# Optimization experiments

Measured on AMD Instinct MI355X. Metric: run time of the kernel, lower is better.

## Reference

```python
import jax, jax.numpy as jnp
import numpy as np

N, E, DIM, NF, ED = 15000, 30000, 64, 3, 1

def _gru_cell(x, h, w_ih, w_hh, b_ih, b_hh):
    gi = x @ w_ih.T + b_ih
    gh = h @ w_hh.T + b_hh
    ir, iz, i_n = jnp.split(gi, 3, axis=-1)
    hr, hz, hn = jnp.split(gh, 3, axis=-1)
    r = jax.nn.sigmoid(ir + hr)
    z = jax.nn.sigmoid(iz + hz)
    n = jnp.tanh(i_n + r * hn)
    return (1.0 - z) * n + z * h

def _lstm_cell(x, h, c, w_ih, w_hh, b_ih, b_hh):
    g = x @ w_ih.T + b_ih + h @ w_hh.T + b_hh
    i, f, gg, o = jnp.split(g, 4, axis=-1)
    c2 = jax.nn.sigmoid(f) * c + jax.nn.sigmoid(i) * jnp.tanh(gg)
    return jax.nn.sigmoid(o) * jnp.tanh(c2), c2

def setup_inputs():
    key = jax.random.key(0)
    ks = jax.random.split(key, 32)
    p = lambda k, shape: jax.random.normal(k, shape, jnp.float32) * 0.05
    return {
        "x": jax.random.normal(ks[0], (N, NF), jnp.float32),
        "edge_index": jax.random.randint(ks[1], (2, E), 0, N),
        "edge_attr": jax.random.uniform(ks[2], (E, ED), jnp.float32),
        "lin0_w": p(ks[3], (DIM, NF)), "lin0_b": p(ks[4], (DIM,)),
        "e1_w": p(ks[5], (DIM, ED)), "e1_b": p(ks[6], (DIM,)),
        "e2_w": p(ks[7], (DIM * DIM, DIM)), "e2_b": p(ks[8], (DIM * DIM,)),
        "root_w": p(ks[9], (DIM, DIM)), "conv_b": p(ks[10], (DIM,)),
        "gru_w_ih": p(ks[11], (3 * DIM, DIM)), "gru_w_hh": p(ks[12], (3 * DIM, DIM)),
        "gru_b_ih": p(ks[13], (3 * DIM,)), "gru_b_hh": p(ks[14], (3 * DIM,)),
        "s2s_w_ih": p(ks[15], (4 * DIM, 2 * DIM)), "s2s_w_hh": p(ks[16], (4 * DIM, DIM)),
        "s2s_b_ih": p(ks[17], (4 * DIM,)), "s2s_b_hh": p(ks[18], (4 * DIM,)),
        "mem_w_ih": p(ks[19], (4 * DIM, 2 * DIM)), "mem_w_hh": p(ks[20], (4 * DIM, DIM)),
        "mem_b_ih": p(ks[21], (4 * DIM,)), "mem_b_hh": p(ks[22], (4 * DIM,)),
        "lin1_w": p(ks[23], (DIM, DIM)), "lin1_b": p(ks[24], (DIM,)),
        "lin3_w": p(ks[25], (1, DIM)), "lin3_b": p(ks[26], (1,)),
    }

def reference(x, edge_index, edge_attr, lin0_w, lin0_b, e1_w, e1_b, e2_w, e2_b,
              root_w, conv_b, gru_w_ih, gru_w_hh, gru_b_ih, gru_b_hh,
              s2s_w_ih, s2s_w_hh, s2s_b_ih, s2s_b_hh,
              mem_w_ih, mem_w_hh, mem_b_ih, mem_b_hh,
              lin1_w, lin1_b, lin3_w, lin3_b):
    n = x.shape[0]
    src, dst = edge_index[0], edge_index[1]
    # per-edge weight matrices from the edge MLP: [E, DIM, DIM] (edge_attr is constant across the 6 conv steps)
    he = jax.nn.relu(edge_attr @ e1_w.T + e1_b)
    We = (he @ e2_w.T + e2_b).reshape(-1, DIM, DIM)
    deg = jax.ops.segment_sum(jnp.ones(src.shape[0], jnp.float32), dst, num_segments=n)
    denom = jnp.maximum(deg, 1.0)[:, None]
    out = jax.nn.relu(x @ lin0_w.T + lin0_b)   # [N, DIM]
    h = out                                    # GRU hidden init = lin0 output
    for _ in range(6):
        msg = jnp.einsum('ei,eio->eo', out[src], We)          # gather + per-edge matmul
        agg = jax.ops.segment_sum(msg, dst, num_segments=n) / denom  # mean aggr
        m = jax.nn.relu(agg + out @ root_w + conv_b)          # NNConv root + bias
        h = _gru_cell(m, h, gru_w_ih, gru_w_hh, gru_b_ih, gru_b_hh)
        out = h
    # Set2Set pooling over a single graph (data.batch is all zeros)
    q_star = jnp.zeros((1, 2 * DIM), x.dtype)
    hs = jnp.zeros((1, DIM), x.dtype)
    cs = jnp.zeros((1, DIM), x.dtype)
    for _ in range(6):
        hs, cs = _lstm_cell(q_star, hs, cs, s2s_w_ih, s2s_w_hh, s2s_b_ih, s2s_b_hh)
        e = out @ hs[0]                     # [N] attention logits
        a = jax.nn.softmax(e)
        r = (a[:, None] * out).sum(0, keepdims=True)  # [1, DIM]
        q_star = jnp.concatenate([hs, r], axis=-1)     # [1, 2*DIM]
    hx, cx = _lstm_cell(q_star, jnp.zeros((1, DIM), x.dtype), jnp.zeros((1, DIM), x.dtype),
                        mem_w_ih, mem_w_hh, mem_b_ih, mem_b_hh)
    o = jax.nn.relu(hx @ lin1_w.T + lin1_b)
    v = o @ lin3_w.T + lin3_b               # [1, 1]
    return v, hx, cx
```

## Files before the change

### kernel.cpp

```cpp
#include <hip/hip_runtime.h>
#include <math.h>

#define Nn 15000
#define NP 15008
#define Ee 30000
#define NB_E 118
#define EB 938

#define OFF_AGG   0
#define OFF_DEG   960512
#define ZERO_END  975520
#define OFF_OUT   975520
#define OFF_DINV  1936032
#define OFF_AT    1951040
#define OFF_BT    2217280
#define OFF_BP    2483520
#define OFF_U     2483584
#define OFF_V     2487744
#define OFF_MC    2491904
#define OFF_PE    2491920
#define OFF_BH    2521920
#define OFF_BC    2529592
#define OFF_SS    2537264
#define OFF_SD    2567264
#define OFF_SA    2597264
#define OFF_SP    2627264
#define OFF_PK    2657264
#define OFF_GMA   2685936
#define OFF_GSA   2686192
#define OFF_GRA   2686448
#define OFF_GMB   2702832
#define OFF_GSB   2703088
#define OFF_GRB   2703344
#define OFF_HS    2719728
#define OFF_CS    2719792
#define OFF_TSA   2719856
#define OFF_TSB   2736240
#define OFF_TMA   2752624
#define OFF_TMB   2769008
#define WS_FLOATS 2785392

__device__ __forceinline__ float sigf(float x) { return 1.0f / (1.0f + expf(-x)); }
__device__ __forceinline__ float bcast(float v, int l) {
    return __int_as_float(__builtin_amdgcn_readlane(__float_as_int(v), l));
}
__device__ __forceinline__ int bcasti(int v, int l) {
    return __builtin_amdgcn_readlane(v, l);
}

__global__ void k_lin0(const float* __restrict__ x, const float* __restrict__ w,
                       const float* __restrict__ b, float* __restrict__ out) {
    int idx = blockIdx.x * 256 + threadIdx.x;
    if (idx >= NP * 64) return;
    int n = idx >> 6, o = idx & 63;
    float v = 0.f;
    if (n < Nn)
        v = fmaxf(b[o] + x[n*3+0]*w[o*3+0] + x[n*3+1]*w[o*3+1] + x[n*3+2]*w[o*3+2], 0.f);
    out[idx] = v;
}

__global__ void k_patterns(const float* __restrict__ e1w, const float* __restrict__ e1b,
                           float* __restrict__ bp, float* __restrict__ u,
                           float* __restrict__ v, int* __restrict__ mc) {
    __shared__ float t[64]; __shared__ int valid[64]; __shared__ float sbp[65]; __shared__ int cnt;
    int k = threadIdx.x;
    float w1 = e1w[k], b1 = e1b[k];
    float tv = 0.f; int va = 0;
    if (w1 != 0.f) { tv = -b1 / w1; va = (tv > 0.f && tv < 1.f) ? 1 : 0; }
    t[k] = tv; valid[k] = va;
    __syncthreads();
    if (va) {
        int rank = 0;
        for (int kk = 0; kk < 64; ++kk)
            if (valid[kk] && (t[kk] < tv || (t[kk] == tv && kk < k))) rank++;
        sbp[rank] = tv;
    }
    if (k == 0) { int c = 0; for (int kk = 0; kk < 64; ++kk) c += valid[kk]; cnt = c; *mc = c; }
    __syncthreads();
    int m = cnt;
    if (k < m) bp[k] = sbp[k];
    for (int j = 0; j <= m; ++j) {
        float lo = (j == 0) ? 0.f : sbp[j-1];
        float hi = (j == m) ? 1.f : sbp[j];
        float c = 0.5f * (lo + hi);
        int msk = (c * w1 + b1) > 0.f;
        u[j*64 + k] = msk ? w1 : 0.f;
        v[j*64 + k] = msk ? b1 : 0.f;
    }
}

__global__ void k_AB2(const float* __restrict__ e2w, const float* __restrict__ e2b,
                      const float* __restrict__ u, const float* __restrict__ v,
                      const int* __restrict__ mc, float* __restrict__ At, float* __restrict__ Bt) {
    int j = blockIdx.x >> 4;
    if (j > *mc) return;
    int qc = blockIdx.x & 15;
    __shared__ float su[64], sv[64];
    if (threadIdx.x < 64) { su[threadIdx.x] = u[j*64+threadIdx.x]; sv[threadIdx.x] = v[j*64+threadIdx.x]; }
    __syncthreads();
    int q = qc*256 + threadIdx.x;
    int i = q >> 6, o = q & 63;
    const float* row = e2w + q*64;
    float a = 0.f, b = 0.f;
    #pragma unroll 8
    for (int k = 0; k < 64; ++k) { float w = row[k]; a = fmaf(su[k], w, a); b = fmaf(sv[k], w, b); }
    At[j*4096 + o*64 + i] = a;
    Bt[j*4096 + o*64 + i] = b + e2b[q];
}

__global__ void k_eprep2(const int* __restrict__ ei, const float* __restrict__ ea,
                         const float* __restrict__ bp, const int* __restrict__ mc,
                         float* __restrict__ deg, int* __restrict__ pe, int* __restrict__ bh) {
    __shared__ int lh[65];
    int tid = threadIdx.x;
    if (tid < 65) lh[tid] = 0;
    __syncthreads();
    int e = blockIdx.x * 256 + tid;
    if (e < Ee) {
        atomicAdd(&deg[ei[Ee + e]], 1.0f);
        float a = ea[e];
        int m = *mc, p = 0;
        for (int j = 0; j < m; ++j) p += (bp[j] <= a) ? 1 : 0;
        pe[e] = p;
        atomicAdd(&lh[p], 1);
    }
    __syncthreads();
    if (tid < 65) bh[blockIdx.x*65 + tid] = lh[tid];
}

__global__ void k_scan2(const float* __restrict__ deg, float* __restrict__ dinv,
                        const int* __restrict__ bh, int* __restrict__ bc) {
    int tid = threadIdx.x;
    if (blockIdx.x < 59) {
        int n = blockIdx.x * 256 + tid;
        if (n < Nn) dinv[n] = 1.0f / fmaxf(deg[n], 1.0f);
        return;
    }
    __shared__ int stot[65]; __shared__ int sbase[65];
    if (tid < 65) {
        int t = 0;
        for (int b = 0; b < NB_E; ++b) t += bh[b*65 + tid];
        stot[tid] = t;
    }
    __syncthreads();
    if (tid == 0) {
        int run = 0;
        for (int j = 0; j < 65; ++j) { sbase[j] = run; run += stot[j]; }
    }
    __syncthreads();
    if (tid < 65) {
        int run = sbase[tid];
        for (int b = 0; b < NB_E; ++b) { bc[b*65 + tid] = run; run += bh[b*65 + tid]; }
    }
}

__global__ void k_scatter2(const int* __restrict__ ei, const float* __restrict__ ea,
                           const int* __restrict__ pe, const int* __restrict__ bc,
                           int* __restrict__ sS, int* __restrict__ sD,
                           float* __restrict__ sA, int* __restrict__ sP) {
    __shared__ int cur[65];
    int tid = threadIdx.x;
    if (tid < 65) cur[tid] = bc[blockIdx.x*65 + tid];
    __syncthreads();
    int e = blockIdx.x * 256 + tid;
    if (e >= Ee) return;
    int p = pe[e];
    int pos = atomicAdd(&cur[p], 1);
    sS[pos] = ei[e]; sD[pos] = ei[Ee + e]; sA[pos] = ea[e]; sP[pos] = p;
}

__global__ void k_wt2(const float* __restrict__ rootw, const float* __restrict__ whh,
                      const float* __restrict__ wih, float* __restrict__ pk) {
    int idx = blockIdx.x * 256 + threadIdx.x;
    if (idx >= 7*4096) return;
    int g = idx >> 12;
    int t = idx & 4095;
    int q4 = t >> 2, k = t & 3;
    int lane = q4 & 63;
    int i4 = q4 >> 6;
    int i = i4*4 + k;
    float v;
    if (g == 0)      v = rootw[i*64 + lane];
    else if (g < 4)  v = whh[((g-1)*64 + lane)*64 + i];
    else             v = wih[((g-4)*64 + lane)*64 + i];
    pk[idx] = v;
}

__global__ void k_wt3(const float* __restrict__ swih, const float* __restrict__ swhh,
                      const float* __restrict__ mwih,
                      float* __restrict__ sa, float* __restrict__ sb,
                      float* __restrict__ ma, float* __restrict__ mb) {
    int idx = blockIdx.x * 256 + threadIdx.x;
    if (idx >= 4*16384) return;
    int t = idx >> 14, r = idx & 16383;
    int i = r >> 8, g = r & 255;
    if (t == 0)      sa[r] = swih[g*128 + i] + swhh[g*64 + i];
    else if (t == 1) sb[r] = swih[g*128 + 64 + i];
    else if (t == 2) ma[r] = mwih[g*128 + i];
    else             mb[r] = mwih[g*128 + 64 + i];
}

__global__ __launch_bounds__(256) void k_edge4(
        const int* __restrict__ sS, const int* __restrict__ sD,
        const float* __restrict__ sA, const int* __restrict__ sP,
        const float* __restrict__ out, const float* __restrict__ At,
        const float* __restrict__ Bt, const float* __restrict__ dinv,
        float* __restrict__ agg) {
    int tid = threadIdx.x, lane = tid & 63;
    int wid = (blockIdx.x * 256 + tid) >> 6;
    const int CH = 8;
    int e0 = wid * CH;
    if (e0 >= Ee) return;
    int e1 = e0 + CH; if (e1 > Ee) e1 = Ee;
    int cnt = e1 - e0;

    int eidx = e0 + lane;
    int msrc = 0, mdst = 0, mp = 0; float ma = 0.f, mdv = 0.f;
    if (lane < cnt) {
        msrc = sS[eidx]; mdst = sD[eidx]; ma = sA[eidx]; mp = sP[eidx];
        mdv = dinv[mdst];
    }

    float Ar[64], Br[64];
    int curp = -1;
    float hv_next = out[bcasti(msrc, 0)*64 + lane];
    for (int j = 0; j < cnt; ++j) {
        float hv = hv_next;
        if (j+1 < cnt) hv_next = out[bcasti(msrc, j+1)*64 + lane];
        int p = bcasti(mp, j);
        if (p != curp) {
            curp = p;
            const float4* Ap4 = (const float4*)(At + p*4096 + lane*64);
            const float4* Bp4 = (const float4*)(Bt + p*4096 + lane*64);
            #pragma unroll
            for (int q = 0; q < 16; ++q) {
                float4 av = Ap4[q], bv = Bp4[q];
                Ar[q*4+0]=av.x; Ar[q*4+1]=av.y; Ar[q*4+2]=av.z; Ar[q*4+3]=av.w;
                Br[q*4+0]=bv.x; Br[q*4+1]=bv.y; Br[q*4+2]=bv.z; Br[q*4+3]=bv.w;
            }
        }
        float a = bcast(ma, j);
        float acc0 = 0.f, acc1 = 0.f;
        #pragma unroll
        for (int i = 0; i < 64; i += 2) {
            float h0 = bcast(hv, i);
            float h1 = bcast(hv, i+1);
            acc0 = fmaf(h0, fmaf(a, Ar[i],   Br[i]),   acc0);
            acc1 = fmaf(h1, fmaf(a, Ar[i+1], Br[i+1]), acc1);
        }
        float acc = (acc0 + acc1) * bcast(mdv, j);
        atomicAdd(&agg[bcasti(mdst, j)*64 + lane], acc);
    }
}

__global__ __launch_bounds__(256, 2) void k_gru8(
        float* __restrict__ out, float* __restrict__ agg,
        const float* __restrict__ pk, const float* __restrict__ convb,
        const float* __restrict__ gbih, const float* __restrict__ gbhh) {
    __shared__ float mL[1024];
    __shared__ float gA[1024];
    __shared__ float gB[1024];
    __shared__ float gC[1024];
    __shared__ float gD[1024];
    int tid = threadIdx.x, lane = tid & 63, w = tid >> 6;
    int pr = w >> 1, hf = w & 1;
    int n0 = blockIdx.x * 16;
    const float4* pk4 = (const float4*)pk;

    float4 wa[16], wb[16];
    {
        int g0 = pr*2, g1 = pr*2 + 1;
        #pragma unroll
        for (int i4 = 0; i4 < 16; ++i4) {
            wa[i4] = pk4[(g0*16 + i4)*64 + lane];
            wb[i4] = pk4[(g1*16 + i4)*64 + lane];
        }
    }
    float cbv = convb[lane];
    int nb0 = n0 + hf*8;

    #pragma unroll
    for (int nb = 0; nb < 8; nb += 4) {
        int n = nb0 + nb;
        float hv0 = out[(n+0)*64 + lane];
        float hv1 = out[(n+1)*64 + lane];
        float hv2 = out[(n+2)*64 + lane];
        float hv3 = out[(n+3)*64 + lane];
        float a0=0.f,a1=0.f,a2=0.f,a3=0.f, b0=0.f,b1=0.f,b2=0.f,b3=0.f;
        #pragma unroll
        for (int i4 = 0; i4 < 16; ++i4) {
            float4 va = wa[i4], vb = wb[i4];
            float h;
            h = bcast(hv0, i4*4+0); a0 = fmaf(h, va.x, a0); b0 = fmaf(h, vb.x, b0);
            h = bcast(hv1, i4*4+0); a1 = fmaf(h, va.x, a1); b1 = fmaf(h, vb.x, b1);
            h = bcast(hv2, i4*4+0); a2 = fmaf(h, va.x, a2); b2 = fmaf(h, vb.x, b2);
            h = bcast(hv3, i4*4+0); a3 = fmaf(h, va.x, a3); b3 = fmaf(h, vb.x, b3);
            h = bcast(hv0, i4*4+1); a0 = fmaf(h, va.y, a0); b0 = fmaf(h, vb.y, b0);
            h = bcast(hv1, i4*4+1); a1 = fmaf(h, va.y, a1); b1 = fmaf(h, vb.y, b1);
            h = bcast(hv2, i4*4+1); a2 = fmaf(h, va.y, a2); b2 = fmaf(h, vb.y, b2);
            h = bcast(hv3, i4*4+1); a3 = fmaf(h, va.y, a3); b3 = fmaf(h, vb.y, b3);
            h = bcast(hv0, i4*4+2); a0 = fmaf(h, va.z, a0); b0 = fmaf(h, vb.z, b0);
            h = bcast(hv1, i4*4+2); a1 = fmaf(h, va.z, a1); b1 = fmaf(h, vb.z, b1);
            h = bcast(hv2, i4*4+2); a2 = fmaf(h, va.z, a2); b2 = fmaf(h, vb.z, b2);
            h = bcast(hv3, i4*4+2); a3 = fmaf(h, va.z, a3); b3 = fmaf(h, vb.z, b3);
            h = bcast(hv0, i4*4+3); a0 = fmaf(h, va.w, a0); b0 = fmaf(h, vb.w, b0);
            h = bcast(hv1, i4*4+3); a1 = fmaf(h, va.w, a1); b1 = fmaf(h, vb.w, b1);
            h = bcast(hv2, i4*4+3); a2 = fmaf(h, va.w, a2); b2 = fmaf(h, vb.w, b2);
            h = bcast(hv3, i4*4+3); a3 = fmaf(h, va.w, a3); b3 = fmaf(h, vb.w, b3);
        }
        int ln = n - n0;
        float fa[4] = {a0,a1,a2,a3}, fb[4] = {b0,b1,b2,b3};
        if (pr == 0) {
            #pragma unroll
            for (int k2 = 0; k2 < 4; ++k2) {
                int gi = (n+k2)*64 + lane;
                float av = agg[gi]; agg[gi] = 0.f;
                mL[(ln+k2)*64 + lane] = fmaxf(fa[k2] + av + cbv, 0.f);
                gA[(ln+k2)*64 + lane] = fb[k2];
            }
        } else {
            #pragma unroll
            for (int k2 = 0; k2 < 4; ++k2) {
                gB[(ln+k2)*64 + lane] = fa[k2];
                gC[(ln+k2)*64 + lane] = fb[k2];
            }
        }
    }
    __syncthreads();

    if (pr == 0) {
        #pragma unroll
        for (int i4 = 0; i4 < 16; ++i4) {
            wa[i4] = pk4[(4*16 + i4)*64 + lane];
            wb[i4] = pk4[(5*16 + i4)*64 + lane];
        }
        float br = gbih[lane]      + gbhh[lane];
        float bz = gbih[64+lane]   + gbhh[64+lane];
        #pragma unroll
        for (int nb = 0; nb < 8; nb += 4) {
            int ln = hf*8 + nb;
            float mv0 = mL[(ln+0)*64 + lane];
            float mv1 = mL[(ln+1)*64 + lane];
            float mv2 = mL[(ln+2)*64 + lane];
            float mv3 = mL[(ln+3)*64 + lane];
            float a0=0.f,a1=0.f,a2=0.f,a3=0.f, b0=0.f,b1=0.f,b2=0.f,b3=0.f;
            #pragma unroll
            for (int i4 = 0; i4 < 16; ++i4) {
                float4 va = wa[i4], vb = wb[i4];
                float h;
                h = bcast(mv0, i4*4+0); a0 = fmaf(h, va.x, a0); b0 = fmaf(h, vb.x, b0);
                h = bcast(mv1, i4*4+0); a1 = fmaf(h, va.x, a1); b1 = fmaf(h, vb.x, b1);
                h = bcast(mv2, i4*4+0); a2 = fmaf(h, va.x, a2); b2 = fmaf(h, vb.x, b2);
                h = bcast(mv3, i4*4+0); a3 = fmaf(h, va.x, a3); b3 = fmaf(h, vb.x, b3);
                h = bcast(mv0, i4*4+1); a0 = fmaf(h, va.y, a0); b0 = fmaf(h, vb.y, b0);
                h = bcast(mv1, i4*4+1); a1 = fmaf(h, va.y, a1); b1 = fmaf(h, vb.y, b1);
                h = bcast(mv2, i4*4+1); a2 = fmaf(h, va.y, a2); b2 = fmaf(h, vb.y, b2);
                h = bcast(mv3, i4*4+1); a3 = fmaf(h, va.y, a3); b3 = fmaf(h, vb.y, b3);
                h = bcast(mv0, i4*4+2); a0 = fmaf(h, va.z, a0); b0 = fmaf(h, vb.z, b0);
                h = bcast(mv1, i4*4+2); a1 = fmaf(h, va.z, a1); b1 = fmaf(h, vb.z, b1);
                h = bcast(mv2, i4*4+2); a2 = fmaf(h, va.z, a2); b2 = fmaf(h, vb.z, b2);
                h = bcast(mv3, i4*4+2); a3 = fmaf(h, va.z, a3); b3 = fmaf(h, vb.z, b3);
                h = bcast(mv0, i4*4+3); a0 = fmaf(h, va.w, a0); b0 = fmaf(h, vb.w, b0);
                h = bcast(mv1, i4*4+3); a1 = fmaf(h, va.w, a1); b1 = fmaf(h, vb.w, b1);
                h = bcast(mv2, i4*4+3); a2 = fmaf(h, va.w, a2); b2 = fmaf(h, vb.w, b2);
                h = bcast(mv3, i4*4+3); a3 = fmaf(h, va.w, a3); b3 = fmaf(h, vb.w, b3);
            }
            float fa[4] = {a0,a1,a2,a3}, fb[4] = {b0,b1,b2,b3};
            #pragma unroll
            for (int k2 = 0; k2 < 4; ++k2) {
                int r4 = (ln+k2)*64 + lane;
                gA[r4] = sigf(fa[k2] + gA[r4] + br);
                gB[r4] = sigf(fb[k2] + gB[r4] + bz);
            }
        }
    } else {
        #pragma unroll
        for (int i4 = 0; i4 < 16; ++i4) wa[i4] = pk4[(6*16 + i4)*64 + lane];
        float bn = gbih[128 + lane];
        #pragma unroll
        for (int nb = 0; nb < 8; nb += 4) {
            int ln = hf*8 + nb;
            float mv0 = mL[(ln+0)*64 + lane];
            float mv1 = mL[(ln+1)*64 + lane];
            float mv2 = mL[(ln+2)*64 + lane];
            float mv3 = mL[(ln+3)*64 + lane];
            float a0=0.f,a1=0.f,a2=0.f,a3=0.f;
            #pragma unroll
            for (int i4 = 0; i4 < 16; ++i4) {
                float4 va = wa[i4];
                float h;
                h = bcast(mv0, i4*4+0); a0 = fmaf(h, va.x, a0);
                h = bcast(mv1, i4*4+0); a1 = fmaf(h, va.x, a1);
                h = bcast(mv2, i4*4+0); a2 = fmaf(h, va.x, a2);
                h = bcast(mv3, i4*4+0); a3 = fmaf(h, va.x, a3);
                h = bcast(mv0, i4*4+1); a0 = fmaf(h, va.y, a0);
                h = bcast(mv1, i4*4+1); a1 = fmaf(h, va.y, a1);
                h = bcast(mv2, i4*4+1); a2 = fmaf(h, va.y, a2);
                h = bcast(mv3, i4*4+1); a3 = fmaf(h, va.y, a3);
                h = bcast(mv0, i4*4+2); a0 = fmaf(h, va.z, a0);
                h = bcast(mv1, i4*4+2); a1 = fmaf(h, va.z, a1);
                h = bcast(mv2, i4*4+2); a2 = fmaf(h, va.z, a2);
                h = bcast(mv3, i4*4+2); a3 = fmaf(h, va.z, a3);
                h = bcast(mv0, i4*4+3); a0 = fmaf(h, va.w, a0);
                h = bcast(mv1, i4*4+3); a1 = fmaf(h, va.w, a1);
                h = bcast(mv2, i4*4+3); a2 = fmaf(h, va.w, a2);
                h = bcast(mv3, i4*4+3); a3 = fmaf(h, va.w, a3);
            }
            float fa[4] = {a0,a1,a2,a3};
            #pragma unroll
            for (int k2 = 0; k2 < 4; ++k2)
                gD[(ln+k2)*64 + lane] = fa[k2] + bn;
        }
    }
    __syncthreads();

    float bhn = gbhh[128 + lane];
    #pragma unroll
    for (int p = 0; p < 4; ++p) {
        int ln = p*4 + w;
        int r4 = ln*64 + lane;
        int gi = (n0 + ln)*64 + lane;
        float r = gA[r4], z = gB[r4];
        float nn = tanhf(fmaf(r, gC[r4] + bhn, gD[r4]));
        float h = out[gi];
        out[gi] = (1.f - z)*nn + z*h;
    }
}

__global__ __launch_bounds__(512) void k_s2s(
        const float* __restrict__ tsa, const float* __restrict__ tsb,
        const float* __restrict__ bih, const float* __restrict__ bhh,
        float* __restrict__ hs, float* __restrict__ cs,
        const float* __restrict__ out,
        const float* __restrict__ gmax_rd, const float* __restrict__ gsum_rd,
        const float* __restrict__ gr_rd,
        float* __restrict__ gmax_wr, float* __restrict__ gsum_wr,
        float* __restrict__ gr_wr, int it) {
    __shared__ float red[512], shs[64], scs[64], srv[64], sg[256];
    __shared__ float sm_m[8], sm_z[8], sm_r[8][64];
    int tid = threadIdx.x, lane = tid & 63, w = tid >> 6;
    if (it == 0) {
        if (tid < 64) { shs[tid] = 0.f; scs[tid] = 0.f; srv[tid] = 0.f; }
    } else {
        float gm = (tid < 256) ? gmax_rd[tid] : -3.4e38f;
        red[tid] = gm; __syncthreads();
        for (int s = 256; s > 0; s >>= 1) { if (tid < s) red[tid] = fmaxf(red[tid], red[tid+s]); __syncthreads(); }
        float M = red[0]; __syncthreads();
        red[tid] = (tid < 256) ? gsum_rd[tid] * expf(gm - M) : 0.f; __syncthreads();
        for (int s = 256; s > 0; s >>= 1) { if (tid < s) red[tid] += red[tid+s]; __syncthreads(); }
        float Z = red[0]; __syncthreads();
        float racc = 0.f;
        for (int b = w; b < 256; b += 8) racc = fmaf(gr_rd[b*64 + lane], expf(gmax_rd[b] - M), racc);
        red[tid] = racc; __syncthreads();
        if (w == 0) {
            float s = 0.f;
            #pragma unroll
            for (int k = 0; k < 8; ++k) s += red[k*64 + lane];
            srv[lane] = s / Z;
        }
        if (tid < 64) { shs[tid] = hs[tid]; scs[tid] = cs[tid]; }
    }
    __syncthreads();
    if (tid < 256) {
        float g = bih[tid] + bhh[tid];
        #pragma unroll 8
        for (int i = 0; i < 64; ++i)
            g += shs[i]*tsa[i*256 + tid] + srv[i]*tsb[i*256 + tid];
        sg[tid] = g;
    }
    __syncthreads();
    if (tid < 64) {
        float ii = sigf(sg[tid]), ff = sigf(sg[64+tid]);
        float gg = tanhf(sg[128+tid]), oo = sigf(sg[192+tid]);
        float c2 = ff*scs[tid] + ii*gg;
        float hn = oo*tanhf(c2);
        shs[tid] = hn;
        if (blockIdx.x == 0) { hs[tid] = hn; cs[tid] = c2; }
    }
    __syncthreads();
    float hsv = shs[lane];
    float m = -3.4e38f, Z2 = 0.f, racc2 = 0.f;
    for (int n = blockIdx.x*8 + w; n < Nn; n += 2048) {
        float ov = out[n*64 + lane];
        float p = ov * hsv;
        #pragma unroll
        for (int off = 32; off > 0; off >>= 1) p += __shfl_xor(p, off, 64);
        float mn = fmaxf(m, p);
        float sc = expf(m - mn);
        float t  = expf(p - mn);
        Z2 = fmaf(Z2, sc, t);
        racc2 = fmaf(racc2, sc, t*ov);
        m = mn;
    }
    if (lane == 0) { sm_m[w] = m; sm_z[w] = Z2; }
    sm_r[w][lane] = racc2;
    __syncthreads();
    if (w == 0) {
        float M = sm_m[0];
        #pragma unroll
        for (int j = 1; j < 8; ++j) M = fmaxf(M, sm_m[j]);
        float Zb = 0.f, rb = 0.f;
        #pragma unroll
        for (int j = 0; j < 8; ++j) {
            float e = expf(sm_m[j] - M);
            Zb = fmaf(sm_z[j], e, Zb);
            rb = fmaf(sm_r[j][lane], e, rb);
        }
        gr_wr[blockIdx.x*64 + lane] = rb;
        if (lane == 0) { gmax_wr[blockIdx.x] = M; gsum_wr[blockIdx.x] = Zb; }
    }
}

__global__ __launch_bounds__(256) void k_final2(
        const float* __restrict__ tma, const float* __restrict__ tmb,
        const float* __restrict__ mbih, const float* __restrict__ mbhh,
        const float* __restrict__ hs,
        const float* __restrict__ gmax, const float* __restrict__ gsum,
        const float* __restrict__ gr,
        const float* __restrict__ l1w, const float* __restrict__ l1b,
        const float* __restrict__ l3w, const float* __restrict__ l3b,
        float* __restrict__ dout) {
    __shared__ float red[256], shs[64], srv[64], sg[256], shx[64], so[64];
    int tid = threadIdx.x, lane = tid & 63, w = tid >> 6;
    {
        float gm = gmax[tid];
        red[tid] = gm; __syncthreads();
        for (int s = 128; s > 0; s >>= 1) { if (tid < s) red[tid] = fmaxf(red[tid], red[tid+s]); __syncthreads(); }
        float M = red[0]; __syncthreads();
        red[tid] = gsum[tid] * expf(gm - M); __syncthreads();
        for (int s = 128; s > 0; s >>= 1) { if (tid < s) red[tid] += red[tid+s]; __syncthreads(); }
        float Z = red[0]; __syncthreads();
        float racc = 0.f;
        for (int b = w; b < 256; b += 4) racc = fmaf(gr[b*64 + lane], expf(gmax[b] - M), racc);
        red[tid] = racc; __syncthreads();
        if (w == 0) srv[lane] = (red[lane] + red[64+lane] + red[128+lane] + red[192+lane]) / Z;
        if (tid < 64) shs[tid] = hs[tid];
    }
    __syncthreads();
    {
        float g = mbih[tid] + mbhh[tid];
        #pragma unroll 8
        for (int i = 0; i < 64; ++i)
            g += shs[i]*tma[i*256 + tid] + srv[i]*tmb[i*256 + tid];
        sg[tid] = g;
    }
    __syncthreads();
    if (tid < 64) {
        float ii = sigf(sg[tid]);
        float gg = tanhf(sg[128+tid]);
        float oo = sigf(sg[192+tid]);
        float c2 = ii * gg;
        float hx = oo * tanhf(c2);
        shx[tid] = hx;
        dout[1 + tid] = hx;
        dout[65 + tid] = c2;
    }
    __syncthreads();
    if (tid < 64) {
        float a = l1b[tid];
        const float* wr = l1w + tid*64;
        #pragma unroll 8
        for (int i = 0; i < 64; ++i) a = fmaf(shx[i], wr[i], a);
        so[tid] = fmaxf(a, 0.f);
    }
    __syncthreads();
    if (tid == 0) {
        float v = l3b[0];
        for (int i = 0; i < 64; ++i) v = fmaf(so[i], l3w[i], v);
        dout[0] = v;
    }
}

extern "C" void kernel_launch(void* const* d_in, const int* in_sizes, int n_in,
                              void* d_out, int out_size, void* d_ws, size_t ws_size,
                              hipStream_t stream) {
    const float* x    = (const float*)d_in[0];
    const int*   ei   = (const int*)  d_in[1];
    const float* ea   = (const float*)d_in[2];
    const float* l0w  = (const float*)d_in[3];
    const float* l0b  = (const float*)d_in[4];
    const float* e1w  = (const float*)d_in[5];
    const float* e1b  = (const float*)d_in[6];
    const float* e2w  = (const float*)d_in[7];
    const float* e2b  = (const float*)d_in[8];
    const float* rootw= (const float*)d_in[9];
    const float* convb= (const float*)d_in[10];
    const float* gwih = (const float*)d_in[11];
    const float* gwhh = (const float*)d_in[12];
    const float* gbih = (const float*)d_in[13];
    const float* gbhh = (const float*)d_in[14];
    const float* swih = (const float*)d_in[15];
    const float* swhh = (const float*)d_in[16];
    const float* sbih = (const float*)d_in[17];
    const float* sbhh = (const float*)d_in[18];
    const float* mwih = (const float*)d_in[19];
    const float* mbih = (const float*)d_in[21];
    const float* mbhh = (const float*)d_in[22];
    const float* l1w  = (const float*)d_in[23];
    const float* l1b  = (const float*)d_in[24];
    const float* l3w  = (const float*)d_in[25];
    const float* l3b  = (const float*)d_in[26];

    float* ws   = (float*)d_ws;
    float* dout = (float*)d_out;
    if (ws_size < (size_t)WS_FLOATS * sizeof(float)) return;

    float* agg  = ws + OFF_AGG;
    float* deg  = ws + OFF_DEG;
    float* out  = ws + OFF_OUT;
    float* dinv = ws + OFF_DINV;
    float* At   = ws + OFF_AT;
    float* Bt   = ws + OFF_BT;
    float* bp   = ws + OFF_BP;
    float* ubuf = ws + OFF_U;
    float* vbuf = ws + OFF_V;
    int*   mc   = (int*)(ws + OFF_MC);
    int*   pe   = (int*)(ws + OFF_PE);
    int*   bh   = (int*)(ws + OFF_BH);
    int*   bc   = (int*)(ws + OFF_BC);
    int*   sS   = (int*)(ws + OFF_SS);
    int*   sD   = (int*)(ws + OFF_SD);
    float* sA   = ws + OFF_SA;
    int*   sP   = (int*)(ws + OFF_SP);
    float* pk   = ws + OFF_PK;
    float* gmA  = ws + OFF_GMA;
    float* gsA  = ws + OFF_GSA;
    float* grA  = ws + OFF_GRA;
    float* gmB  = ws + OFF_GMB;
    float* gsB  = ws + OFF_GSB;
    float* grB  = ws + OFF_GRB;
    float* hs   = ws + OFF_HS;
    float* cs   = ws + OFF_CS;
    float* tsa  = ws + OFF_TSA;
    float* tsb  = ws + OFF_TSB;
    float* tma  = ws + OFF_TMA;
    float* tmb  = ws + OFF_TMB;

    hipMemsetAsync(d_ws, 0, (size_t)ZERO_END * sizeof(float), stream);

    k_lin0    <<<(NP*64 + 255)/256, 256, 0, stream>>>(x, l0w, l0b, out);
    k_patterns<<<1, 64, 0, stream>>>(e1w, e1b, bp, ubuf, vbuf, mc);
    k_AB2     <<<65*16, 256, 0, stream>>>(e2w, e2b, ubuf, vbuf, mc, At, Bt);
    k_eprep2  <<<NB_E, 256, 0, stream>>>(ei, ea, bp, mc, deg, pe, bh);
    k_scan2   <<<60, 256, 0, stream>>>(deg, dinv, bh, bc);
    k_scatter2<<<NB_E, 256, 0, stream>>>(ei, ea, pe, bc, sS, sD, sA, sP);
    k_wt2     <<<(7*4096 + 255)/256, 256, 0, stream>>>(rootw, gwhh, gwih, pk);
    k_wt3     <<<(4*16384 + 255)/256, 256, 0, stream>>>(swih, swhh, mwih, tsa, tsb, tma, tmb);

    for (int s = 0; s < 6; ++s) {
        k_edge4<<<EB, 256, 0, stream>>>(sS, sD, sA, sP, out, At, Bt, dinv, agg);
        k_gru8 <<<NP/16, 256, 0, stream>>>(out, agg, pk, convb, gbih, gbhh);
    }

    for (int it = 0; it < 6; ++it) {
        float* gm_rd = (it & 1) ? gmA : gmB;
        float* gs_rd = (it & 1) ? gsA : gsB;
        float* gr_rd = (it & 1) ? grA : grB;
        float* gm_wr = (it & 1) ? gmB : gmA;
        float* gs_wr = (it & 1) ? gsB : gsA;
        float* gr_wr = (it & 1) ? grB : grA;
        k_s2s<<<256, 512, 0, stream>>>(tsa, tsb, sbih, sbhh, hs, cs, out,
                                       gm_rd, gs_rd, gr_rd, gm_wr, gs_wr, gr_wr, it);
    }

    k_final2<<<1, 256, 0, stream>>>(tma, tmb, mbih, mbhh, hs, gmB, gsB, grB,
                                    l1w, l1b, l3w, l3b, dout);
}
```

Measured before the change: 510.3 us.

## Restructure GRU kernel to stage all weights in LDS with 8 nodes per wave

The GRU update kernel now copies all seven 64x64 packed weight matrices (112 KB) into shared memory once per block. Each wave then processes 8 nodes end to end, computing root, hidden-gate and input-gate products from LDS with no intermediate shared-memory gate buffers and no mid-kernel barriers. Node padding grows to a multiple of 64 and the workspace offsets shift to match. The goal is to amortise weight loads over more nodes and drop the cross-wave handoff, at the cost of a large per-block LDS copy, lower occupancy and higher register pressure from the 8-node accumulators.

Result: faster. 453.2 us (-11.2%).

```diff
diff --git a/kernel.cpp b/kernel.cpp
--- a/kernel.cpp
+++ b/kernel.cpp
@@ -2,43 +2,43 @@
 #include <math.h>
 
 #define Nn 15000
-#define NP 15008
+#define NP 15040
 #define Ee 30000
 #define NB_E 118
 #define EB 938
 
 #define OFF_AGG   0
-#define OFF_DEG   960512
-#define ZERO_END  975520
-#define OFF_OUT   975520
-#define OFF_DINV  1936032
-#define OFF_AT    1951040
-#define OFF_BT    2217280
-#define OFF_BP    2483520
-#define OFF_U     2483584
-#define OFF_V     2487744
-#define OFF_MC    2491904
-#define OFF_PE    2491920
-#define OFF_BH    2521920
-#define OFF_BC    2529592
-#define OFF_SS    2537264
-#define OFF_SD    2567264
-#define OFF_SA    2597264
-#define OFF_SP    2627264
-#define OFF_PK    2657264
-#define OFF_GMA   2685936
-#define OFF_GSA   2686192
-#define OFF_GRA   2686448
-#define OFF_GMB   2702832
-#define OFF_GSB   2703088
-#define OFF_GRB   2703344
-#define OFF_HS    2719728
-#define OFF_CS    2719792
-#define OFF_TSA   2719856
-#define OFF_TSB   2736240
-#define OFF_TMA   2752624
-#define OFF_TMB   2769008
-#define WS_FLOATS 2785392
+#define OFF_DEG   962560
+#define ZERO_END  977560
+#define OFF_OUT   977568
+#define OFF_DINV  1940128
+#define OFF_AT    1955136
+#define OFF_BT    2221376
+#define OFF_BP    2487616
+#define OFF_U     2487680
+#define OFF_V     2491840
+#define OFF_MC    2496000
+#define OFF_PE    2496016
+#define OFF_BH    2526016
+#define OFF_BC    2533696
+#define OFF_SS    2541376
+#define OFF_SD    2571376
+#define OFF_SA    2601376
+#define OFF_SP    2631376
+#define OFF_PK    2661376
+#define OFF_GMA   2690048
+#define OFF_GSA   2690304
+#define OFF_GRA   2690560
+#define OFF_GMB   2706944
+#define OFF_GSB   2707200
+#define OFF_GRB   2707456
+#define OFF_HS    2723840
+#define OFF_CS    2723904
+#define OFF_TSA   2723968
+#define OFF_TSB   2740352
+#define OFF_TMA   2756736
+#define OFF_TMB   2773120
+#define WS_FLOATS 2789504
 
 __device__ __forceinline__ float sigf(float x) { return 1.0f / (1.0f + expf(-x)); }
 __device__ __forceinline__ float bcast(float v, int l) {
@@ -253,177 +253,92 @@
     }
 }
 
-__global__ __launch_bounds__(256, 2) void k_gru8(
+__global__ __launch_bounds__(512, 2) void k_gru9(
         float* __restrict__ out, float* __restrict__ agg,
         const float* __restrict__ pk, const float* __restrict__ convb,
         const float* __restrict__ gbih, const float* __restrict__ gbhh) {
-    __shared__ float mL[1024];
-    __shared__ float gA[1024];
-    __shared__ float gB[1024];
-    __shared__ float gC[1024];
-    __shared__ float gD[1024];
+    __shared__ __align__(16) float wL[7*4096];
     int tid = threadIdx.x, lane = tid & 63, w = tid >> 6;
-    int pr = w >> 1, hf = w & 1;
-    int n0 = blockIdx.x * 16;
-    const float4* pk4 = (const float4*)pk;
-
-    float4 wa[16], wb[16];
     {
-        int g0 = pr*2, g1 = pr*2 + 1;
-        #pragma unroll
-        for (int i4 = 0; i4 < 16; ++i4) {
-            wa[i4] = pk4[(g0*16 + i4)*64 + lane];
-            wb[i4] = pk4[(g1*16 + i4)*64 + lane];
+        const float4* src = (const float4*)pk;
+        float4* dst = (float4*)wL;
+        #pragma unroll
+        for (int i = 0; i < 14; ++i) dst[i*512 + tid] = src[i*512 + tid];
+    }
+    __syncthreads();
+    const float4* wL4 = (const float4*)wL;
+    int n0 = blockIdx.x*64 + w*8;
+
+    float hv[8], mv[8], ghr[8], ghz[8], ghn[8];
+    #pragma unroll
+    for (int k = 0; k < 8; ++k) hv[k] = out[(n0+k)*64 + lane];
+
+    float a0[8], a1[8], a2[8], a3[8];
+    #pragma unroll
+    for (int k = 0; k < 8; ++k) { a0[k]=0.f; a1[k]=0.f; a2[k]=0.f; a3[k]=0.f; }
+    #pragma unroll 4
+    for (int i4 = 0; i4 < 16; ++i4) {
+        float4 w0 = wL4[(0*16+i4)*64 + lane];
+        float4 w1 = wL4[(1*16+i4)*64 + lane];
+        float4 w2 = wL4[(2*16+i4)*64 + lane];
+        float4 w3 = wL4[(3*16+i4)*64 + lane];
+        #pragma unroll
+        for (int k = 0; k < 8; ++k) {
+            float h;
+            h = bcast(hv[k], i4*4+0);
+            a0[k]=fmaf(h,w0.x,a0[k]); a1[k]=fmaf(h,w1.x,a1[k]);
+            a2[k]=fmaf(h,w2.x,a2[k]); a3[k]=fmaf(h,w3.x,a3[k]);
+            h = bcast(hv[k], i4*4+1);
+            a0[k]=fmaf(h,w0.y,a0[k]); a1[k]=fmaf(h,w1.y,a1[k]);
+            a2[k]=fmaf(h,w2.y,a2[k]); a3[k]=fmaf(h,w3.y,a3[k]);
+            h = bcast(hv[k], i4*4+2);
+            a0[k]=fmaf(h,w0.z,a0[k]); a1[k]=fmaf(h,w1.z,a1[k]);
+            a2[k]=fmaf(h,w2.z,a2[k]); a3[k]=fmaf(h,w3.z,a3[k]);
+            h = bcast(hv[k], i4*4+3);
+            a0[k]=fmaf(h,w0.w,a0[k]); a1[k]=fmaf(h,w1.w,a1[k]);
+            a2[k]=fmaf(h,w2.w,a2[k]); a3[k]=fmaf(h,w3.w,a3[k]);
         }
     }
     float cbv = convb[lane];
-    int nb0 = n0 + hf*8;
-
     #pragma unroll
-    for (int nb = 0; nb < 8; nb += 4) {
-        int n = nb0 + nb;
-        float hv0 = out[(n+0)*64 + lane];
-        float hv1 = out[(n+1)*64 + lane];
-        float hv2 = out[(n+2)*64 + lane];
-        float hv3 = out[(n+3)*64 + lane];
-        float a0=0.f,a1=0.f,a2=0.f,a3=0.f, b0=0.f,b1=0.f,b2=0.f,b3=0.f;
-        #pragma unroll
-        for (int i4 = 0; i4 < 16; ++i4) {
-            float4 va = wa[i4], vb = wb[i4];
+    for (int k = 0; k < 8; ++k) {
+        int gi = (n0+k)*64 + lane;
+        float av = agg[gi]; agg[gi] = 0.f;
+        mv[k] = fmaxf(a0[k] + av + cbv, 0.f);
+        ghr[k] = a1[k]; ghz[k] = a2[k]; ghn[k] = a3[k];
+    }
+
+    #pragma unroll
+    for (int k = 0; k < 8; ++k) { a0[k]=0.f; a1[k]=0.f; a2[k]=0.f; }
+    #pragma unroll 4
+    for (int i4 = 0; i4 < 16; ++i4) {
+        float4 w4v = wL4[(4*16+i4)*64 + lane];
+        float4 w5v = wL4[(5*16+i4)*64 + lane];
+        float4 w6v = wL4[(6*16+i4)*64 + lane];
+        #pragma unroll
+        for (int k = 0; k < 8; ++k) {
             float h;
-            h = bcast(hv0, i4*4+0); a0 = fmaf(h, va.x, a0); b0 = fmaf(h, vb.x, b0);
-            h = bcast(hv1, i4*4+0); a1 = fmaf(h, va.x, a1); b1 = fmaf(h, vb.x, b1);
-            h = bcast(hv2, i4*4+0); a2 = fmaf(h, va.x, a2); b2 = fmaf(h, vb.x, b2);
-            h = bcast(hv3, i4*4+0); a3 = fmaf(h, va.x, a3); b3 = fmaf(h, vb.x, b3);
-            h = bcast(hv0, i4*4+1); a0 = fmaf(h, va.y, a0); b0 = fmaf(h, vb.y, b0);
-            h = bcast(hv1, i4*4+1); a1 = fmaf(h, va.y, a1); b1 = fmaf(h, vb.y, b1);
-            h = bcast(hv2, i4*4+1); a2 = fmaf(h, va.y, a2); b2 = fmaf(h, vb.y, b2);
-            h = bcast(hv3, i4*4+1); a3 = fmaf(h, va.y, a3); b3 = fmaf(h, vb.y, b3);
-            h = bcast(hv0, i4*4+2); a0 = fmaf(h, va.z, a0); b0 = fmaf(h, vb.z, b0);
-            h = bcast(hv1, i4*4+2); a1 = fmaf(h, va.z, a1); b1 = fmaf(h, vb.z, b1);
-            h = bcast(hv2, i4*4+2); a2 = fmaf(h, va.z, a2); b2 = fmaf(h, vb.z, b2);
-            h = bcast(hv3, i4*4+2); a3 = fmaf(h, va.z, a3); b3 = fmaf(h, vb.z, b3);
-            h = bcast(hv0, i4*4+3); a0 = fmaf(h, va.w, a0); b0 = fmaf(h, vb.w, b0);
-            h = bcast(hv1, i4*4+3); a1 = fmaf(h, va.w, a1); b1 = fmaf(h, vb.w, b1);
-            h = bcast(hv2, i4*4+3); a2 = fmaf(h, va.w, a2); b2 = fmaf(h, vb.w, b2);
-            h = bcast(hv3, i4*4+3); a3 = fmaf(h, va.w, a3); b3 = fmaf(h, vb.w, b3);
+            h = bcast(mv[k], i4*4+0);
+            a0[k]=fmaf(h,w4v.x,a0[k]); a1[k]=fmaf(h,w5v.x,a1[k]); a2[k]=fmaf(h,w6v.x,a2[k]);
+            h = bcast(mv[k], i4*4+1);
+            a0[k]=fmaf(h,w4v.y,a0[k]); a1[k]=fmaf(h,w5v.y,a1[k]); a2[k]=fmaf(h,w6v.y,a2[k]);
+            h = bcast(mv[k], i4*4+2);
+            a0[k]=fmaf(h,w4v.z,a0[k]); a1[k]=fmaf(h,w5v.z,a1[k]); a2[k]=fmaf(h,w6v.z,a2[k]);
+            h = bcast(mv[k], i4*4+3);
+            a0[k]=fmaf(h,w4v.w,a0[k]); a1[k]=fmaf(h,w5v.w,a1[k]); a2[k]=fmaf(h,w6v.w,a2[k]);
         }
-        int ln = n - n0;
-        float fa[4] = {a0,a1,a2,a3}, fb[4] = {b0,b1,b2,b3};
-        if (pr == 0) {
-            #pragma unroll
-            for (int k2 = 0; k2 < 4; ++k2) {
-                int gi = (n+k2)*64 + lane;
-                float av = agg[gi]; agg[gi] = 0.f;
-                mL[(ln+k2)*64 + lane] = fmaxf(fa[k2] + av + cbv, 0.f);
-                gA[(ln+k2)*64 + lane] = fb[k2];
-            }
-        } else {
-            #pragma unroll
-            for (int k2 = 0; k2 < 4; ++k2) {
-                gB[(ln+k2)*64 + lane] = fa[k2];
-                gC[(ln+k2)*64 + lane] = fb[k2];
-            }
-        }
-    }
-    __syncthreads();
-
-    if (pr == 0) {
-        #pragma unroll
-        for (int i4 = 0; i4 < 16; ++i4) {
-            wa[i4] = pk4[(4*16 + i4)*64 + lane];
-            wb[i4] = pk4[(5*16 + i4)*64 + lane];
-        }
-        float br = gbih[lane]      + gbhh[lane];
-        float bz = gbih[64+lane]   + gbhh[64+lane];
-        #pragma unroll
-        for (int nb = 0; nb < 8; nb += 4) {
-            int ln = hf*8 + nb;
-            float mv0 = mL[(ln+0)*64 + lane];
-            float mv1 = mL[(ln+1)*64 + lane];
-            float mv2 = mL[(ln+2)*64 + lane];
-            float mv3 = mL[(ln+3)*64 + lane];
-            float a0=0.f,a1=0.f,a2=0.f,a3=0.f, b0=0.f,b1=0.f,b2=0.f,b3=0.f;
-            #pragma unroll
-            for (int i4 = 0; i4 < 16; ++i4) {
-                float4 va = wa[i4], vb = wb[i4];
-                float h;
-                h = bcast(mv0, i4*4+0); a0 = fmaf(h, va.x, a0); b0 = fmaf(h, vb.x, b0);
-                h = bcast(mv1, i4*4+0); a1 = fmaf(h, va.x, a1); b1 = fmaf(h, vb.x, b1);
-                h = bcast(mv2, i4*4+0); a2 = fmaf(h, va.x, a2); b2 = fmaf(h, vb.x, b2);
-                h = bcast(mv3, i4*4+0); a3 = fmaf(h, va.x, a3); b3 = fmaf(h, vb.x, b3);
-                h = bcast(mv0, i4*4+1); a0 = fmaf(h, va.y, a0); b0 = fmaf(h, vb.y, b0);
-                h = bcast(mv1, i4*4+1); a1 = fmaf(h, va.y, a1); b1 = fmaf(h, vb.y, b1);
-                h = bcast(mv2, i4*4+1); a2 = fmaf(h, va.y, a2); b2 = fmaf(h, vb.y, b2);
-                h = bcast(mv3, i4*4+1); a3 = fmaf(h, va.y, a3); b3 = fmaf(h, vb.y, b3);
-                h = bcast(mv0, i4*4+2); a0 = fmaf(h, va.z, a0); b0 = fmaf(h, vb.z, b0);
-                h = bcast(mv1, i4*4+2); a1 = fmaf(h, va.z, a1); b1 = fmaf(h, vb.z, b1);
-                h = bcast(mv2, i4*4+2); a2 = fmaf(h, va.z, a2); b2 = fmaf(h, vb.z, b2);
-                h = bcast(mv3, i4*4+2); a3 = fmaf(h, va.z, a3); b3 = fmaf(h, vb.z, b3);
-                h = bcast(mv0, i4*4+3); a0 = fmaf(h, va.w, a0); b0 = fmaf(h, vb.w, b0);
-                h = bcast(mv1, i4*4+3); a1 = fmaf(h, va.w, a1); b1 = fmaf(h, vb.w, b1);
-                h = bcast(mv2, i4*4+3); a2 = fmaf(h, va.w, a2); b2 = fmaf(h, vb.w, b2);
-                h = bcast(mv3, i4*4+3); a3 = fmaf(h, va.w, a3); b3 = fmaf(h, vb.w, b3);
-            }
-            float fa[4] = {a0,a1,a2,a3}, fb[4] = {b0,b1,b2,b3};
-            #pragma unroll
-            for (int k2 = 0; k2 < 4; ++k2) {
-                int r4 = (ln+k2)*64 + lane;
-                gA[r4] = sigf(fa[k2] + gA[r4] + br);
-                gB[r4] = sigf(fb[k2] + gB[r4] + bz);
-            }
-        }
-    } else {
-        #pragma unroll
-        for (int i4 = 0; i4 < 16; ++i4) wa[i4] = pk4[(6*16 + i4)*64 + lane];
-        float bn = gbih[128 + lane];
-        #pragma unroll
-        for (int nb = 0; nb < 8; nb += 4) {
-            int ln = hf*8 + nb;
-            float mv0 = mL[(ln+0)*64 + lane];
-            float mv1 = mL[(ln+1)*64 + lane];
-            float mv2 = mL[(ln+2)*64 + lane];
-            float mv3 = mL[(ln+3)*64 + lane];
-            float a0=0.f,a1=0.f,a2=0.f,a3=0.f;
-            #pragma unroll
-            for (int i4 = 0; i4 < 16; ++i4) {
-                float4 va = wa[i4];
-                float h;
-                h = bcast(mv0, i4*4+0); a0 = fmaf(h, va.x, a0);
-                h = bcast(mv1, i4*4+0); a1 = fmaf(h, va.x, a1);
-                h = bcast(mv2, i4*4+0); a2 = fmaf(h, va.x, a2);
-                h = bcast(mv3, i4*4+0); a3 = fmaf(h, va.x, a3);
-                h = bcast(mv0, i4*4+1); a0 = fmaf(h, va.y, a0);
-                h = bcast(mv1, i4*4+1); a1 = fmaf(h, va.y, a1);
-                h = bcast(mv2, i4*4+1); a2 = fmaf(h, va.y, a2);
-                h = bcast(mv3, i4*4+1); a3 = fmaf(h, va.y, a3);
-                h = bcast(mv0, i4*4+2); a0 = fmaf(h, va.z, a0);
-                h = bcast(mv1, i4*4+2); a1 = fmaf(h, va.z, a1);
-                h = bcast(mv2, i4*4+2); a2 = fmaf(h, va.z, a2);
-                h = bcast(mv3, i4*4+2); a3 = fmaf(h, va.z, a3);
-                h = bcast(mv0, i4*4+3); a0 = fmaf(h, va.w, a0);
-                h = bcast(mv1, i4*4+3); a1 = fmaf(h, va.w, a1);
-                h = bcast(mv2, i4*4+3); a2 = fmaf(h, va.w, a2);
-                h = bcast(mv3, i4*4+3); a3 = fmaf(h, va.w, a3);
-            }
-            float fa[4] = {a0,a1,a2,a3};
-            #pragma unroll
-            for (int k2 = 0; k2 < 4; ++k2)
-                gD[(ln+k2)*64 + lane] = fa[k2] + bn;
-        }
-    }
-    __syncthreads();
-
-    float bhn = gbhh[128 + lane];
+    }
+
+    float br  = gbih[lane]      + gbhh[lane];
+    float bz  = gbih[64+lane]   + gbhh[64+lane];
+    float bnI = gbih[128+lane];
+    float bnH = gbhh[128+lane];
     #pragma unroll
-    for (int p = 0; p < 4; ++p) {
-        int ln = p*4 + w;
-        int r4 = ln*64 + lane;
-        int gi = (n0 + ln)*64 + lane;
-        float r = gA[r4], z = gB[r4];
-        float nn = tanhf(fmaf(r, gC[r4] + bhn, gD[r4]));
-        float h = out[gi];
-        out[gi] = (1.f - z)*nn + z*h;
+    for (int k = 0; k < 8; ++k) {
+        float r  = sigf(a0[k] + ghr[k] + br);
+        float z  = sigf(a1[k] + ghz[k] + bz);
+        float nn = tanhf(fmaf(r, ghn[k] + bnH, a2[k] + bnI));
+        out[(n0+k)*64 + lane] = (1.f - z)*nn + z*hv[k];
     }
 }
 
@@ -649,7 +564,7 @@
 
     for (int s = 0; s < 6; ++s) {
         k_edge4<<<EB, 256, 0, stream>>>(sS, sD, sA, sP, out, At, Bt, dinv, agg);
-        k_gru8 <<<NP/16, 256, 0, stream>>>(out, agg, pk, convb, gbih, gbhh);
+        k_gru9 <<<NP/64, 512, 0, stream>>>(out, agg, pk, convb, gbih, gbhh);
     }
 
     for (int it = 0; it < 6; ++it) {
```
